# Optimization experiments

Hardware: AMD Instinct MI355X
Metric: run time of the kernel (lower is better)

The kernel has to match this reference:

```python
import jax, jax.numpy as jnp
import numpy as np

L = 8        # num_layers
REPEAT = 2   # repeats per layer
DIM = 256    # mixer hidden dim
DIM2 = 128   # head dim (divisible by 32 for AvgPool1d(32))
B = 8192
EPS = 1e-5


def hardswish(x):
    return x * jnp.clip(x + 3.0, 0.0, 6.0) * (1.0 / 6.0)


def layernorm(x, g, b):
    m = jnp.mean(x, axis=-1, keepdims=True)
    xc = x - m
    v = jnp.mean(xc * xc, axis=-1, keepdims=True)
    return xc * jax.lax.rsqrt(v + EPS) * g + b


def setup_inputs() -> dict:
    key = jax.random.key(0)
    ks = jax.random.split(key, 32)
    s = 0.1
    inp = {
        "x": jax.random.normal(ks[0], (B, 3, 32, 32), dtype=jnp.float32),
        "conv_w": jax.random.normal(ks[1], (3,), dtype=jnp.float32) * s,
        "conv_b": jax.random.normal(ks[2], (1,), dtype=jnp.float32) * s,
        "fc0_w": jax.random.normal(ks[3], (32, 32), dtype=jnp.float32) * s,
        "fc0_b": jax.random.normal(ks[4], (32,), dtype=jnp.float32) * s,
        "ln1_g": jnp.ones((L, 32), dtype=jnp.float32),
        "ln1_b": jnp.zeros((L, 32), dtype=jnp.float32),
        "w11": jax.random.normal(ks[5], (L, DIM, 32), dtype=jnp.float32) * s,
        "b11": jax.random.normal(ks[6], (L, DIM), dtype=jnp.float32) * s,
        "w12": jax.random.normal(ks[7], (L, 32, DIM), dtype=jnp.float32) * s,
        "b12": jax.random.normal(ks[8], (L, 32), dtype=jnp.float32) * s,
        "ln2_g": jnp.ones((L, 32), dtype=jnp.float32),
        "ln2_b": jnp.zeros((L, 32), dtype=jnp.float32),
        "w21": jax.random.normal(ks[9], (L, DIM, 32), dtype=jnp.float32) * s,
        "b21": jax.random.normal(ks[10], (L, DIM), dtype=jnp.float32) * s,
        "w22": jax.random.normal(ks[11], (L, 32, DIM), dtype=jnp.float32) * s,
        "b22": jax.random.normal(ks[12], (L, 32), dtype=jnp.float32) * s,
        "fc1_w": jax.random.normal(ks[13], (DIM2, 32), dtype=jnp.float32) * s,
        "fc1_b": jax.random.normal(ks[14], (DIM2,), dtype=jnp.float32) * s,
        "fcout_w": jax.random.normal(ks[15], (10, DIM2), dtype=jnp.float32) * s,
        "fcout_b": jax.random.normal(ks[16], (10,), dtype=jnp.float32) * s,
    }
    return inp


def reference(x, conv_w, conv_b, fc0_w, fc0_b, ln1_g, ln1_b, w11, b11, w12, b12,
              ln2_g, ln2_b, w21, b21, w22, b22, fc1_w, fc1_b, fcout_w, fcout_b):
    # rgb_conv: 1x1 conv 3->1 channels, then squeeze -> [B, 32, 32]
    h = jnp.einsum('bchw,c->bhw', x, conv_w) + conv_b[0]
    h = h @ fc0_w.T + fc0_b  # fc0 over last dim (32)

    for i in range(L):
        for _ in range(REPEAT):
            # token-mixing branch (operates along dim 1 via permute)
            t = layernorm(h, ln1_g[i], ln1_b[i])
            t = jnp.swapaxes(t, 1, 2)                      # [B, 32, 32]
            t = hardswish(t @ w11[i].T + b11[i])           # [B, 32, DIM]
            t = t @ w12[i].T + b12[i]                      # [B, 32, 32]
            h = h + jnp.swapaxes(t, 1, 2)
            # channel-mixing branch
            c = layernorm(h, ln2_g[i], ln2_b[i])
            c = hardswish(c @ w21[i].T + b21[i])           # [B, 32, DIM]
            h = h + (c @ w22[i].T + b22[i])                # [B, 32, 32]

    y = hardswish(h @ fc1_w.T + fc1_b)                     # [B, 32, DIM2]
    # AvgPool1d(kernel=32, stride=32) over last dim -> [B, 32, DIM2//32]
    y = y.reshape(y.shape[0], 32, DIM2 // 32, 32).mean(axis=-1)
    y = y.reshape(y.shape[0], -1)                          # [B, DIM2]
    return y @ fcout_w.T + fcout_b                         # [B, 10]
```

## Files before the change

### kernel.cpp

```cpp
#include <hip/hip_runtime.h>

#define LNUM 8

typedef __attribute__((ext_vector_type(4))) float f32x4;
typedef __attribute__((ext_vector_type(2))) float f32x2;
typedef __attribute__((ext_vector_type(8))) _Float16 f16x8;
typedef __attribute__((ext_vector_type(2))) _Float16 f16x2;

#define MFMAH(A,B,C) __builtin_amdgcn_mfma_f32_16x16x32_f16(A,B,C,0,0,0)

#define PKRTZ(a,b) __builtin_bit_cast(f16x2, __builtin_amdgcn_cvt_pkrtz(a,b))

__device__ __forceinline__ float hswish_clamp(float t) {
  return __builtin_amdgcn_fmed3f(t + 3.f, 0.f, 6.f);
}

__device__ __forceinline__ int hws(int row, int c) {
  return (row << 5) + ((((c >> 2) ^ (row & 7)) << 2) | (c & 3));
}

__global__ void prep_weights(const float* __restrict__ w11, const float* __restrict__ b11,
                             const float* __restrict__ w12, const float* __restrict__ b12,
                             const float* __restrict__ g1,  const float* __restrict__ be1,
                             const float* __restrict__ w21, const float* __restrict__ b21,
                             const float* __restrict__ w22, const float* __restrict__ b22,
                             const float* __restrict__ g2,  const float* __restrict__ be2,
                             char* __restrict__ ws)
{
  const int lb = blockIdx.x;
  const int lay = lb >> 1, br = lb & 1;
  const float* w1  = (br ? w21 : w11) + lay*8192;
  const float* w2  = (br ? w22 : w12) + lay*8192;
  const float* bb1 = (br ? b21 : b11) + lay*256;
  const float* bb2 = (br ? b22 : b12) + lay*32;
  const float* gg  = (br ? g2  : g1 ) + lay*32;
  const float* bb  = (br ? be2 : be1) + lay*32;
  char* o = ws + (size_t)lb * 34816;
  _Float16* w1f = (_Float16*)o;
  _Float16* w2f = (_Float16*)(o + 16384);
  float* pr  = (float*)(o + 32768);
  const int t = threadIdx.x;
  #pragma unroll
  for (int i = 0; i < 4; ++i) {
    int s = t + i*256;
    int lane = s & 63;
    int row = (s >> 6)*16 + (lane & 15);
    int kb  = ((lane >> 4) & 3) * 8;
    const float* src = w1 + row*32 + kb;
    #pragma unroll
    for (int j = 0; j < 8; ++j) w1f[s*8 + j] = (_Float16)src[j];
  }
  #pragma unroll
  for (int i = 0; i < 4; ++i) {
    int s = t + i*256;
    int lane = s & 63;
    int tt = s >> 7;
    int nt = (s >> 6) & 1;
    int n  = nt*16 + (lane & 15);
    int qq = (lane >> 4) & 3;
    const float* src = w2 + n*256 + tt*32 + qq*4;
    _Float16* dst = w2f + s*8;
    #pragma unroll
    for (int j = 0; j < 4; ++j) dst[j]     = (_Float16)(src[j]      * (1.0f/6.0f));
    #pragma unroll
    for (int j = 0; j < 4; ++j) dst[4 + j] = (_Float16)(src[16 + j] * (1.0f/6.0f));
  }
  pr[t] = bb1[t];
  if (t < 32)      pr[256 + t] = bb2[t];
  else if (t < 64) pr[256 + t] = gg[t - 32];
  else if (t < 96) pr[256 + t] = bb[t - 64];
}

__global__ __launch_bounds__(256, 4)
void mixer_mfma(const float* __restrict__ x,
                const float* __restrict__ conv_w, const float* __restrict__ conv_b,
                const float* __restrict__ fc0_w,  const float* __restrict__ fc0_b,
                const char*  __restrict__ ws,
                const float* __restrict__ fc1_w,  const float* __restrict__ fc1_b,
                const float* __restrict__ fcout_w, const float* __restrict__ fcout_b,
                float* __restrict__ out)
{
  __shared__ float smem[4 * 2176];
  const int tid = threadIdx.x;
  const int wv  = tid >> 6;
  const int lid = tid & 63;
  const int ml  = lid & 15;
  const int q   = lid >> 4;
  const int q4  = q << 2, q8 = q << 3;
  const int sl  = lid >> 5, r = lid & 31;
  const int r7  = r & 7;

  float* hW  = smem + wv * 2176;
  float* stW = hW + 2048;

  const size_t b0 = (size_t)blockIdx.x * 8 + (size_t)wv * 2;

  {
    const size_t b = b0 + sl;
    const float* xb = x + b*3072 + r*32;
    const float cw0 = conv_w[0], cw1 = conv_w[1], cw2 = conv_w[2], cb = conv_b[0];
    float g[32];
    #pragma unroll
    for (int j4 = 0; j4 < 8; ++j4) {
      f32x4 a0 = *(const f32x4*)(xb + j4*4);
      f32x4 a1 = *(const f32x4*)(xb + 1024 + j4*4);
      f32x4 a2 = *(const f32x4*)(xb + 2048 + j4*4);
      #pragma unroll
      for (int e = 0; e < 4; ++e)
        g[j4*4+e] = cw0*a0[e] + cw1*a1[e] + cw2*a2[e] + cb;
    }
    f32x4* hp = (f32x4*)(hW + sl*1024 + (r << 5));
    #pragma unroll
    for (int a = 0; a < 8; ++a) {
      f32x4 w;
      #pragma unroll
      for (int e = 0; e < 4; ++e) {
        const int j = a*4 + e;
        const float* wr = fc0_w + j*32;
        float acc = fc0_b[j];
        #pragma unroll
        for (int k = 0; k < 32; ++k) acc += g[k]*wr[k];
        w[e] = acc;
      }
      hp[a ^ r7] = w;
    }
  }

  for (int lay = 0; lay < LNUM; ++lay)
  for (int rep = 0; rep < 2; ++rep)
  for (int br = 0; br < 2; ++br) {
    const char* wsb = ws + (size_t)(lay*2 + br) * 34816;
    const f16x8* w1f = (const f16x8*)wsb;
    const f16x8* w2f = (const f16x8*)(wsb + 16384);
    const float* pb1 = (const float*)(wsb + 32768);
    const float* pb2 = pb1 + 256;
    const float* pg  = pb1 + 288;
    const float* pbt = pb1 + 320;

    {
      const f32x4* hp = (const f32x4*)(hW + sl*1024 + (r << 5));
      float sum = 0.f, sq = 0.f;
      #pragma unroll
      for (int a = 0; a < 8; ++a) {
        f32x4 v = hp[a ^ r7];
        #pragma unroll
        for (int e = 0; e < 4; ++e) { sum += v[e]; sq += v[e]*v[e]; }
      }
      float m = sum * (1.f/32.f);
      float rstd = rsqrtf(sq*(1.f/32.f) - m*m + 1e-5f);
      *(f32x2*)(stW + ((sl << 5) + r)*2) = (f32x2){m, rstd};
    }

    f16x8 b1[4];
    if (br == 0) {
      const float ga = pg[ml],  gb = pg[16 + ml];
      const float ba = pbt[ml], bb2v = pbt[16 + ml];
      #pragma unroll
      for (int i = 0; i < 8; ++i) {
        const int k = q8 + i;
        f32x2 s0 = *(const f32x2*)(stW + k*2);
        f32x2 s1 = *(const f32x2*)(stW + 64 + k*2);
        #pragma unroll
        for (int mt = 0; mt < 4; ++mt) {
          const int samp = mt >> 1;
          const int c = ((mt & 1) << 4) + ml;
          f32x2 st = samp ? s1 : s0;
          float v = hW[samp*1024 + hws(k, c)];
          float g_ = (mt & 1) ? gb : ga;
          float be = (mt & 1) ? bb2v : ba;
          b1[mt][i] = (_Float16)((v - st[0]) * st[1] * g_ + be);
        }
      }
    } else {
      f32x4 g0 = *(const f32x4*)(pg + q8);
      f32x4 g1 = *(const f32x4*)(pg + q8 + 4);
      f32x4 t0 = *(const f32x4*)(pbt + q8);
      f32x4 t1 = *(const f32x4*)(pbt + q8 + 4);
      #pragma unroll
      for (int mt = 0; mt < 4; ++mt) {
        const int samp = mt >> 1;
        const int row = ((mt & 1) << 4) + ml;
        f32x2 st = *(const f32x2*)(stW + ((samp << 5) + row)*2);
        const f32x4* hr = (const f32x4*)(hW + samp*1024 + (row << 5));
        f32x4 v0 = hr[(2*q)     ^ (row & 7)];
        f32x4 v1 = hr[(2*q + 1) ^ (row & 7)];
        #pragma unroll
        for (int e = 0; e < 4; ++e) {
          b1[mt][e]     = (_Float16)((v0[e] - st[0]) * st[1] * g0[e] + t0[e]);
          b1[mt][4 + e] = (_Float16)((v1[e] - st[0]) * st[1] * g1[e] + t1[e]);
        }
      }
    }

    f32x4 acc2[2][4];
    {
      f32x4 i0 = *(const f32x4*)(pb2 + q4);
      f32x4 i1 = *(const f32x4*)(pb2 + 16 + q4);
      #pragma unroll
      for (int mt = 0; mt < 4; ++mt) { acc2[0][mt] = i0; acc2[1][mt] = i1; }
    }
    #pragma unroll 2
    for (int t = 0; t < 8; ++t) {
      f16x8 a1a = w1f[(t*2 + 0)*64 + lid];
      f16x8 a1b = w1f[(t*2 + 1)*64 + lid];
      f32x4 biasa = *(const f32x4*)(pb1 + t*32 + q4);
      f32x4 biasb = *(const f32x4*)(pb1 + t*32 + 16 + q4);
      f16x8 a2a = w2f[(t*2 + 0)*64 + lid];
      f16x8 a2b = w2f[(t*2 + 1)*64 + lid];
      #pragma unroll
      for (int mt = 0; mt < 4; ++mt) {
        f32x4 c1a = MFMAH(a1a, b1[mt], biasa);
        f32x4 c1b = MFMAH(a1b, b1[mt], biasb);
        float va0 = c1a[0]*hswish_clamp(c1a[0]);
        float va1 = c1a[1]*hswish_clamp(c1a[1]);
        float va2 = c1a[2]*hswish_clamp(c1a[2]);
        float va3 = c1a[3]*hswish_clamp(c1a[3]);
        float vb0 = c1b[0]*hswish_clamp(c1b[0]);
        float vb1 = c1b[1]*hswish_clamp(c1b[1]);
        float vb2 = c1b[2]*hswish_clamp(c1b[2]);
        float vb3 = c1b[3]*hswish_clamp(c1b[3]);
        union { f16x2 h2[4]; f16x8 v; } b2u;
        b2u.h2[0] = PKRTZ(va0, va1);
        b2u.h2[1] = PKRTZ(va2, va3);
        b2u.h2[2] = PKRTZ(vb0, vb1);
        b2u.h2[3] = PKRTZ(vb2, vb3);
        acc2[0][mt] = MFMAH(a2a, b2u.v, acc2[0][mt]);
        acc2[1][mt] = MFMAH(a2b, b2u.v, acc2[1][mt]);
      }
    }

    if (br == 0) {
      #pragma unroll
      for (int mt = 0; mt < 4; ++mt) {
        const int samp = mt >> 1;
        const int c = ((mt & 1) << 4) + ml;
        float* hs = hW + samp*1024;
        #pragma unroll
        for (int nt = 0; nt < 2; ++nt)
        #pragma unroll
        for (int rg = 0; rg < 4; ++rg) {
          const int n = (nt << 4) + q4 + rg;
          hs[hws(n, c)] += acc2[nt][mt][rg];
        }
      }
    } else {
      #pragma unroll
      for (int mt = 0; mt < 4; ++mt) {
        const int samp = mt >> 1;
        const int row = ((mt & 1) << 4) + ml;
        f32x4* hr = (f32x4*)(hW + samp*1024 + (row << 5));
        #pragma unroll
        for (int nt = 0; nt < 2; ++nt) {
          const int a = ((nt << 2) + q) ^ (row & 7);
          f32x4 v = hr[a];
          v += acc2[nt][mt];
          hr[a] = v;
        }
      }
    }
  }

  {
    const size_t b = b0 + sl;
    float hv[32];
    {
      const f32x4* hp = (const f32x4*)(hW + sl*1024 + (r << 5));
      #pragma unroll
      for (int a = 0; a < 8; ++a) {
        f32x4 v = hp[a ^ r7];
        #pragma unroll
        for (int e = 0; e < 4; ++e) hv[a*4 + e] = v[e];
      }
    }
    float pooled[4];
    #pragma unroll
    for (int c = 0; c < 4; ++c) {
      float accp = 0.f;
      for (int e2 = 0; e2 < 32; ++e2) {
        const float* wr = fc1_w + (c*32 + e2)*32;
        float acc = fc1_b[c*32 + e2];
        #pragma unroll
        for (int k = 0; k < 32; ++k) acc += hv[k]*wr[k];
        accp += acc * hswish_clamp(acc) * (1.f/6.f);
      }
      pooled[c] = accp * (1.f/32.f);
    }
    float* pf = hW + sl*1024;
    #pragma unroll
    for (int c = 0; c < 4; ++c) pf[r*4 + c] = pooled[c];
    if (r < 10) {
      const float* pv = hW + sl*1024;
      const float* wr = fcout_w + r*128;
      float acc = fcout_b[r];
      #pragma unroll 8
      for (int m = 0; m < 128; ++m) acc += pv[m]*wr[m];
      out[b*10 + r] = acc;
    }
  }
}

extern "C" void kernel_launch(void* const* d_in, const int* in_sizes, int n_in,
                              void* d_out, int out_size, void* d_ws, size_t ws_size,
                              hipStream_t stream) {
  (void)in_sizes; (void)n_in; (void)out_size; (void)ws_size;
  const float* x       = (const float*)d_in[0];
  const float* conv_w  = (const float*)d_in[1];
  const float* conv_b  = (const float*)d_in[2];
  const float* fc0_w   = (const float*)d_in[3];
  const float* fc0_b   = (const float*)d_in[4];
  const float* ln1_g   = (const float*)d_in[5];
  const float* ln1_b   = (const float*)d_in[6];
  const float* w11     = (const float*)d_in[7];
  const float* b11     = (const float*)d_in[8];
  const float* w12     = (const float*)d_in[9];
  const float* b12     = (const float*)d_in[10];
  const float* ln2_g   = (const float*)d_in[11];
  const float* ln2_b   = (const float*)d_in[12];
  const float* w21     = (const float*)d_in[13];
  const float* b21     = (const float*)d_in[14];
  const float* w22     = (const float*)d_in[15];
  const float* b22     = (const float*)d_in[16];
  const float* fc1_w   = (const float*)d_in[17];
  const float* fc1_b   = (const float*)d_in[18];
  const float* fcout_w = (const float*)d_in[19];
  const float* fcout_b = (const float*)d_in[20];
  float* out = (float*)d_out;
  char* ws = (char*)d_ws;

  prep_weights<<<16, 256, 0, stream>>>(w11, b11, w12, b12, ln1_g, ln1_b,
                                       w21, b21, w22, b22, ln2_g, ln2_b, ws);
  mixer_mfma<<<1024, 256, 0, stream>>>(x, conv_w, conv_b, fc0_w, fc0_b,
                                       (const char*)ws, fc1_w, fc1_b,
                                       fcout_w, fcout_b, out);
}
```

Measured before the change: 487.2 us.

## Move fc1 head onto fp16 MFMA, pack hardswish in half2, lower launch bound

Converts fc1 weights to fp16 in MFMA fragment layout in an extra prep block. The final fc1 and hardswish-pool stage now runs as MFMA tiles with cross-lane shuffles instead of a scalar per-thread 32x128 dot loop. The mixer hardswish is computed on packed half2 values after conversion, which changes rounding slightly. Launch bounds drop from 4 to 3 waves per SIMD, which allows more registers but may reduce occupancy.

```diff
diff --git a/kernel.cpp b/kernel.cpp
--- a/kernel.cpp
+++ b/kernel.cpp
@@ -8,11 +8,18 @@
 typedef __attribute__((ext_vector_type(2))) _Float16 f16x2;
 
 #define MFMAH(A,B,C) __builtin_amdgcn_mfma_f32_16x16x32_f16(A,B,C,0,0,0)
-
 #define PKRTZ(a,b) __builtin_bit_cast(f16x2, __builtin_amdgcn_cvt_pkrtz(a,b))
 
 __device__ __forceinline__ float hswish_clamp(float t) {
   return __builtin_amdgcn_fmed3f(t + 3.f, 0.f, 6.f);
+}
+__device__ __forceinline__ f16x2 hsw_pk(f16x2 t) {
+  const f16x2 c3 = {(_Float16)3.0f, (_Float16)3.0f};
+  const f16x2 c0 = {(_Float16)0.0f, (_Float16)0.0f};
+  const f16x2 c6 = {(_Float16)6.0f, (_Float16)6.0f};
+  f16x2 u = t + c3;
+  u = __builtin_elementwise_min(__builtin_elementwise_max(u, c0), c6);
+  return t * u;
 }
 
 __device__ __forceinline__ int hws(int row, int c) {
@@ -25,9 +32,28 @@
                              const float* __restrict__ w21, const float* __restrict__ b21,
                              const float* __restrict__ w22, const float* __restrict__ b22,
                              const float* __restrict__ g2,  const float* __restrict__ be2,
+                             const float* __restrict__ fc1w, const float* __restrict__ fc1b,
                              char* __restrict__ ws)
 {
   const int lb = blockIdx.x;
+  const int t = threadIdx.x;
+  if (lb == 16) {
+    char* o = ws + (size_t)16 * 34816;
+    _Float16* wf = (_Float16*)o;
+    float* pr = (float*)(o + 8192);
+    #pragma unroll
+    for (int i = 0; i < 2; ++i) {
+      int s = t + i*256;
+      int lane = s & 63;
+      int row = (s >> 6)*16 + (lane & 15);
+      int kb  = ((lane >> 4) & 3) * 8;
+      const float* src = fc1w + row*32 + kb;
+      #pragma unroll
+      for (int j = 0; j < 8; ++j) wf[s*8 + j] = (_Float16)src[j];
+    }
+    if (t < 128) pr[t] = fc1b[t];
+    return;
+  }
   const int lay = lb >> 1, br = lb & 1;
   const float* w1  = (br ? w21 : w11) + lay*8192;
   const float* w2  = (br ? w22 : w12) + lay*8192;
@@ -39,7 +65,6 @@
   _Float16* w1f = (_Float16*)o;
   _Float16* w2f = (_Float16*)(o + 16384);
   float* pr  = (float*)(o + 32768);
-  const int t = threadIdx.x;
   #pragma unroll
   for (int i = 0; i < 4; ++i) {
     int s = t + i*256;
@@ -71,12 +96,11 @@
   else if (t < 96) pr[256 + t] = bb[t - 64];
 }
 
-__global__ __launch_bounds__(256, 4)
+__global__ __launch_bounds__(256, 3)
 void mixer_mfma(const float* __restrict__ x,
                 const float* __restrict__ conv_w, const float* __restrict__ conv_b,
                 const float* __restrict__ fc0_w,  const float* __restrict__ fc0_b,
                 const char*  __restrict__ ws,
-                const float* __restrict__ fc1_w,  const float* __restrict__ fc1_b,
                 const float* __restrict__ fcout_w, const float* __restrict__ fcout_b,
                 float* __restrict__ out)
 {
@@ -211,19 +235,11 @@
       for (int mt = 0; mt < 4; ++mt) {
         f32x4 c1a = MFMAH(a1a, b1[mt], biasa);
         f32x4 c1b = MFMAH(a1b, b1[mt], biasb);
-        float va0 = c1a[0]*hswish_clamp(c1a[0]);
-        float va1 = c1a[1]*hswish_clamp(c1a[1]);
-        float va2 = c1a[2]*hswish_clamp(c1a[2]);
-        float va3 = c1a[3]*hswish_clamp(c1a[3]);
-        float vb0 = c1b[0]*hswish_clamp(c1b[0]);
-        float vb1 = c1b[1]*hswish_clamp(c1b[1]);
-        float vb2 = c1b[2]*hswish_clamp(c1b[2]);
-        float vb3 = c1b[3]*hswish_clamp(c1b[3]);
         union { f16x2 h2[4]; f16x8 v; } b2u;
-        b2u.h2[0] = PKRTZ(va0, va1);
-        b2u.h2[1] = PKRTZ(va2, va3);
-        b2u.h2[2] = PKRTZ(vb0, vb1);
-        b2u.h2[3] = PKRTZ(vb2, vb3);
+        b2u.h2[0] = hsw_pk(PKRTZ(c1a[0], c1a[1]));
+        b2u.h2[1] = hsw_pk(PKRTZ(c1a[2], c1a[3]));
+        b2u.h2[2] = hsw_pk(PKRTZ(c1b[0], c1b[1]));
+        b2u.h2[3] = hsw_pk(PKRTZ(c1b[2], c1b[3]));
         acc2[0][mt] = MFMAH(a2a, b2u.v, acc2[0][mt]);
         acc2[1][mt] = MFMAH(a2b, b2u.v, acc2[1][mt]);
       }
@@ -261,40 +277,63 @@
   }
 
   {
-    const size_t b = b0 + sl;
-    float hv[32];
-    {
-      const f32x4* hp = (const f32x4*)(hW + sl*1024 + (r << 5));
-      #pragma unroll
-      for (int a = 0; a < 8; ++a) {
-        f32x4 v = hp[a ^ r7];
-        #pragma unroll
-        for (int e = 0; e < 4; ++e) hv[a*4 + e] = v[e];
-      }
-    }
-    float pooled[4];
-    #pragma unroll
-    for (int c = 0; c < 4; ++c) {
-      float accp = 0.f;
-      for (int e2 = 0; e2 < 32; ++e2) {
-        const float* wr = fc1_w + (c*32 + e2)*32;
-        float acc = fc1_b[c*32 + e2];
-        #pragma unroll
-        for (int k = 0; k < 32; ++k) acc += hv[k]*wr[k];
-        accp += acc * hswish_clamp(acc) * (1.f/6.f);
-      }
-      pooled[c] = accp * (1.f/32.f);
-    }
-    float* pf = hW + sl*1024;
-    #pragma unroll
-    for (int c = 0; c < 4; ++c) pf[r*4 + c] = pooled[c];
+    const f16x8* fc1f = (const f16x8*)(ws + (size_t)16 * 34816);
+    const float* fb   = (const float*)(ws + (size_t)16 * 34816 + 8192);
+    f16x8 be[4];
+    #pragma unroll
+    for (int mt = 0; mt < 4; ++mt) {
+      const int samp = mt >> 1;
+      const int row = ((mt & 1) << 4) + ml;
+      const f32x4* hr = (const f32x4*)(hW + samp*1024 + (row << 5));
+      f32x4 v0 = hr[(2*q)     ^ (row & 7)];
+      f32x4 v1 = hr[(2*q + 1) ^ (row & 7)];
+      #pragma unroll
+      for (int e = 0; e < 4; ++e) {
+        be[mt][e]     = (_Float16)v0[e];
+        be[mt][4 + e] = (_Float16)v1[e];
+      }
+    }
+    float pl[4][4] = {};
+    #pragma unroll
+    for (int dt = 0; dt < 8; ++dt) {
+      f16x8 af = fc1f[dt*64 + lid];
+      f32x4 bias4 = *(const f32x4*)(fb + dt*16 + q4);
+      #pragma unroll
+      for (int mt = 0; mt < 4; ++mt) {
+        f32x4 c = MFMAH(af, be[mt], bias4);
+        float s = 0.f;
+        #pragma unroll
+        for (int rg = 0; rg < 4; ++rg) s += c[rg] * hswish_clamp(c[rg]);
+        pl[dt >> 1][mt] += s;
+      }
+    }
+    #pragma unroll
+    for (int t = 0; t < 4; ++t)
+    #pragma unroll
+    for (int mt = 0; mt < 4; ++mt) {
+      float v = pl[t][mt];
+      v += __shfl_xor(v, 16);
+      v += __shfl_xor(v, 32);
+      pl[t][mt] = v;
+    }
+    if (q == 0) {
+      #pragma unroll
+      for (int mt = 0; mt < 4; ++mt)
+      #pragma unroll
+      for (int t = 0; t < 4; ++t)
+        hW[(mt >> 1)*1024 + (((mt & 1) << 4) + ml)*4 + t] = pl[t][mt];
+    }
     if (r < 10) {
       const float* pv = hW + sl*1024;
       const float* wr = fcout_w + r*128;
-      float acc = fcout_b[r];
-      #pragma unroll 8
-      for (int m = 0; m < 128; ++m) acc += pv[m]*wr[m];
-      out[b*10 + r] = acc;
+      float acc = 0.f;
+      #pragma unroll
+      for (int m4 = 0; m4 < 32; ++m4) {
+        f32x4 p4 = *(const f32x4*)(pv + m4*4);
+        f32x4 w4 = *(const f32x4*)(wr + m4*4);
+        acc += p4[0]*w4[0] + p4[1]*w4[1] + p4[2]*w4[2] + p4[3]*w4[3];
+      }
+      out[(b0 + sl)*10 + r] = fcout_b[r] + acc * (1.f/192.f);
     }
   }
 }
@@ -327,9 +366,9 @@
   float* out = (float*)d_out;
   char* ws = (char*)d_ws;
 
-  prep_weights<<<16, 256, 0, stream>>>(w11, b11, w12, b12, ln1_g, ln1_b,
-                                       w21, b21, w22, b22, ln2_g, ln2_b, ws);
+  prep_weights<<<17, 256, 0, stream>>>(w11, b11, w12, b12, ln1_g, ln1_b,
+                                       w21, b21, w22, b22, ln2_g, ln2_b,
+                                       fc1_w, fc1_b, ws);
   mixer_mfma<<<1024, 256, 0, stream>>>(x, conv_w, conv_b, fc0_w, fc0_b,
-                                       (const char*)ws, fc1_w, fc1_b,
-                                       fcout_w, fcout_b, out);
-}
+                                       (const char*)ws, fcout_w, fcout_b, out);
+}
```

Result: faster. 430.5 us (-11.6%).
